# Kernel tuning notes

Measured on AMD Instinct MI355X. Metric: run time of the kernel, lower is better.

## Reference

```python
import jax, jax.numpy as jnp
import numpy as np

B, N, NP, NS = 8, 4096, 1024, 32
CF = 64            # input point-feature channels; in_channel = 3 + CF = 67
MLP = [64, 128, 256]
EPS = 1e-5         # BatchNorm eps (torch default)


def setup_inputs() -> dict:
    key = jax.random.key(0)
    ks = jax.random.split(key, 8)
    inp = {
        "xyz": jax.random.normal(ks[0], (B, N, 3), jnp.float32),
        "points": jax.random.normal(ks[1], (B, CF, N), jnp.float32),
        "sample_idx": jax.random.randint(ks[2], (B, NP), 0, N, dtype=jnp.int32),
        "neighbor_idx": jax.random.randint(ks[3], (B, NP, NS), 0, N, dtype=jnp.int32),
    }
    c = 3 + CF
    for i, o in enumerate(MLP):
        wk = jax.random.fold_in(ks[4], i)
        inp[f"W{i}"] = jax.random.normal(wk, (o, c), jnp.float32) * (1.0 / np.sqrt(c))
        inp[f"b{i}"] = jnp.zeros((o,), jnp.float32)
        inp[f"gamma{i}"] = jnp.ones((o,), jnp.float32)
        inp[f"beta{i}"] = jnp.zeros((o,), jnp.float32)
        c = o
    return inp


def _forward(xyz, points, sample_idx, neighbor_idx, params):
    # xyz: (B,N,3)  points: (B,CF,N)
    new_xyz = jnp.take_along_axis(xyz, sample_idx[:, :, None], axis=1)        # (B,NP,3)
    nbr_xyz = jax.vmap(lambda x, idx: x[idx])(xyz, neighbor_idx)               # (B,NP,NS,3)
    rel = nbr_xyz - new_xyz[:, :, None, :]                                     # (B,NP,NS,3)
    nbr_feat = jax.vmap(lambda f, idx: f[:, idx])(points, neighbor_idx)        # (B,CF,NP,NS)
    x = jnp.concatenate([rel.transpose(0, 3, 1, 2), nbr_feat], axis=1)         # (B,3+CF,NP,NS)
    # 1x1 Conv2d -> BatchNorm2d (training-mode batch stats) -> ReLU stack
    for W, b, g, be in params:
        x = jnp.einsum('oc,bcps->bops', W, x) + b[None, :, None, None]
        mu = x.mean(axis=(0, 2, 3), keepdims=True)
        var = x.var(axis=(0, 2, 3), keepdims=True)
        x = g[None, :, None, None] * (x - mu) * jax.lax.rsqrt(var + EPS) + be[None, :, None, None]
        x = jax.nn.relu(x)
    new_points = x.max(axis=-1)                                                # (B,C_out,NP)
    return new_xyz, new_points


def reference(xyz, points, sample_idx, neighbor_idx,
              W0, b0, gamma0, beta0,
              W1, b1, gamma1, beta1,
              W2, b2, gamma2, beta2):
    params = [(W0, b0, gamma0, beta0), (W1, b1, gamma1, beta1), (W2, b2, gamma2, beta2)]
    return _forward(xyz, points, sample_idx, neighbor_idx, params)
```

## Files before the change

kernel.cpp:

```cpp
#include <hip/hip_runtime.h>

typedef unsigned short u16;
typedef unsigned int u32;
typedef __attribute__((ext_vector_type(8))) short short8;
typedef __attribute__((ext_vector_type(16))) float f32x16;

#define BB 8
#define NN 4096
#define NPP 1024
#define NSS 32
#define CFF 64
#define C0 67
#define H0 64
#define H1 128
#define H2 256
#define MTOT (BB*NPP*NSS)
#define BN_EPS 1e-5f
#define INV_M (1.0f/262144.0f)

#define MFMA32(a,b,c) __builtin_amdgcn_mfma_f32_32x32x16_bf16(a,b,c,0,0,0)

__device__ __forceinline__ float bf2f(u16 h){ return __uint_as_float(((u32)h)<<16); }
__device__ __forceinline__ u16 f2bf(float f){
  u32 u = __float_as_uint(f);
  u32 r = (u + 0x7fffu + ((u>>16)&1u)) >> 16;
  return (u16)r;
}
__device__ __forceinline__ u32 pack2(float a, float b){
  return (u32)f2bf(a) | ((u32)f2bf(b)<<16);
}

#define WS_NEED 46280704u

__global__ __launch_bounds__(256) void k_setup(
    const float* __restrict__ xyz, const float* __restrict__ points,
    const int* __restrict__ sidx,
    const float* __restrict__ W0, const float* __restrict__ W1, const float* __restrict__ W2,
    u16* __restrict__ ptsT, u16* __restrict__ Wt0c, u16* __restrict__ Wt1c,
    u16* __restrict__ Wt2c, float* __restrict__ out_newxyz)
{
  int blk = blockIdx.x, tid = threadIdx.x;
  if (blk < 512) {
    __shared__ float t[64][65];
    int b = blk >> 6, n0 = (blk & 63) << 6;
    int nloc = tid & 63, cpart = tid >> 6;
    for (int i = 0; i < 16; ++i) {
      int c = i*4 + cpart;
      t[c][nloc] = points[(size_t)(b*CFF + c)*NN + n0 + nloc];
    }
    __syncthreads();
    int cloc = tid & 63, npart = tid >> 6;
    for (int i = 0; i < 16; ++i) {
      int n = i*4 + npart;
      ptsT[((size_t)(b*NN + n0 + n))*CFF + cloc] = f2bf(t[cloc][n]);
    }
  } else if (blk < 544) {
    int t0 = (blk - 512)*256 + tid;
    int b = t0 >> 10;
    int s = sidx[t0];
    for (int k = 0; k < 3; ++k)
      out_newxyz[(size_t)t0*3 + k] = xyz[((size_t)(b*NN + s))*3 + k];
  } else if (blk == 544) {
    for (int i = 0; i < 24; ++i) {
      int e = i*256 + tid;
      int kc = e >> 9, o = (e >> 3) & 63, j = e & 7, k = kc*8 + j;
      float v = (k < 64) ? W0[o*C0 + 3 + k] : ((k < 67) ? W0[o*C0 + (k - 64)] : 0.f);
      Wt0c[e] = f2bf(v);
    }
  } else if (blk == 545) {
    for (int i = 0; i < 32; ++i) {
      int e = i*256 + tid;
      int kc = e >> 10, n = (e >> 3) & 127, j = e & 7;
      Wt1c[e] = f2bf(W1[n*H0 + kc*8 + j]);
    }
  } else {
    int base = (blk - 546) * 4096;
    for (int i = 0; i < 16; ++i) {
      int e = base + i*256 + tid;
      int kc = e >> 11, n = (e >> 3) & 255, j = e & 7;
      Wt2c[e] = f2bf(W2[n*H1 + kc*8 + j]);
    }
  }
}

__global__ __launch_bounds__(256) void k_xyz_only(
    const float* __restrict__ xyz, const int* __restrict__ sidx, float* __restrict__ out_newxyz)
{
  int t0 = blockIdx.x*256 + threadIdx.x;
  int b = t0 >> 10;
  int s = sidx[t0];
  for (int k = 0; k < 3; ++k)
    out_newxyz[(size_t)t0*3 + k] = xyz[((size_t)(b*NN + s))*3 + k];
}

__global__ __launch_bounds__(256) void k_l0(
    const float* __restrict__ xyz, const int* __restrict__ sidx, const int* __restrict__ nidx,
    const u16* __restrict__ ptsT, const u16* __restrict__ Wt0c,
    u16* __restrict__ y0, float* __restrict__ stats)
{
  __shared__ u16 XLc[12*128*8];
  __shared__ u16 W0c[12*64*8];
  int tid = threadIdx.x;
  int m0 = blockIdx.x * 128;
  int b = m0 >> 15;

  for (int i = 0; i < 3; ++i)
    ((uint4*)W0c)[i*256 + tid] = ((const uint4*)Wt0c)[i*256 + tid];

  int pos = tid & 127, half = tid >> 7;
  int m = m0 + pos;
  int nb = nidx[m];
  {
    const uint4* prow = (const uint4*)(ptsT + ((size_t)(b*NN + nb))*CFF + half*32);
    uint4 h0 = prow[0], h1 = prow[1], h2 = prow[2], h3 = prow[3];
    *(uint4*)&XLc[((half*4+0)*128 + pos)*8] = h0;
    *(uint4*)&XLc[((half*4+1)*128 + pos)*8] = h1;
    *(uint4*)&XLc[((half*4+2)*128 + pos)*8] = h2;
    *(uint4*)&XLc[((half*4+3)*128 + pos)*8] = h3;
    if (half == 0) {
      int p = (m & 32767) >> 5;
      int sp = sidx[b*NPP + p];
      float r0 = xyz[((size_t)(b*NN+nb))*3+0] - xyz[((size_t)(b*NN+sp))*3+0];
      float r1 = xyz[((size_t)(b*NN+nb))*3+1] - xyz[((size_t)(b*NN+sp))*3+1];
      float r2 = xyz[((size_t)(b*NN+nb))*3+2] - xyz[((size_t)(b*NN+sp))*3+2];
      uint4 v = { pack2(r0, r1), pack2(r2, 0.f), 0u, 0u };
      *(uint4*)&XLc[(8*128 + pos)*8] = v;
    } else {
      uint4 z = {0u,0u,0u,0u};
      *(uint4*)&XLc[(9*128 + pos)*8]  = z;
      *(uint4*)&XLc[(10*128 + pos)*8] = z;
      *(uint4*)&XLc[(11*128 + pos)*8] = z;
    }
  }
  __syncthreads();

  int lane = tid & 63, wv = tid >> 6;
  int l31 = lane & 31, kh = lane >> 5;
  int nt = wv & 1, mtb = (wv >> 1) * 2;
  f32x16 acc[2];
  for (int mi = 0; mi < 2; ++mi) for (int r = 0; r < 16; ++r) acc[mi][r] = 0.f;

  for (int kt = 0; kt < 6; ++kt) {
    int ck = kt*2 + kh;
    short8 bfrag = *(const short8*)&W0c[(ck*64 + nt*32 + l31)*8];
    for (int mi = 0; mi < 2; ++mi) {
      short8 afrag = *(const short8*)&XLc[(ck*128 + (mtb+mi)*32 + l31)*8];
      acc[mi] = MFMA32(afrag, bfrag, acc[mi]);
    }
  }

  float s = 0.f, q = 0.f;
  for (int mi = 0; mi < 2; ++mi)
    for (int r = 0; r < 16; ++r) { float y = acc[mi][r]; s += y; q += y*y; }
  s += __shfl_xor(s, 32); q += __shfl_xor(q, 32);
  if (lane < 32) {
    int slot = blockIdx.x & 7;
    atomicAdd(&stats[slot*256 + nt*32 + lane], s);
    atomicAdd(&stats[2048 + slot*256 + nt*32 + lane], q);
  }
  for (int mi = 0; mi < 2; ++mi)
    for (int r = 0; r < 16; ++r) {
      int mm = (mtb+mi)*32 + (r&3) + 8*(r>>2) + 4*kh;
      y0[(size_t)(m0+mm)*H0 + nt*32 + l31] = f2bf(acc[mi][r]);
    }
}

__global__ __launch_bounds__(256) void k_l1s(
    const u16* __restrict__ y0, const u16* __restrict__ Wt1c,
    const float* __restrict__ g0, const float* __restrict__ e0,
    const float* __restrict__ stIn, float* __restrict__ stOut)
{
  __shared__ u16 X0c[8*128*8];
  __shared__ u16 W1c[8*128*8];
  __shared__ float scl0[64], sft0[64];
  int tid = threadIdx.x;
  int m0 = blockIdx.x * 128;

  if (tid < 64) {
    float s = 0.f, q = 0.f;
    for (int sl = 0; sl < 8; ++sl) { s += stIn[sl*256 + tid]; q += stIn[2048 + sl*256 + tid]; }
    float mu = s*INV_M, var = q*INV_M - mu*mu;
    float sc = g0[tid] * rsqrtf(var + BN_EPS);
    scl0[tid] = sc; sft0[tid] = e0[tid] - mu*sc;
  }
  for (int i = 0; i < 4; ++i)
    ((uint4*)W1c)[i*256 + tid] = ((const uint4*)Wt1c)[i*256 + tid];

  int pos = tid & 127, half = tid >> 7;
  {
    const u16* row = y0 + (size_t)(m0 + pos)*H0 + half*32;
    u16 hs[32];
    for (int t = 0; t < 4; ++t) *(uint4*)&hs[t*8] = ((const uint4*)row)[t];
    __syncthreads();
    u16 ob[32];
    for (int j = 0; j < 32; ++j) {
      int c = half*32 + j;
      ob[j] = f2bf(fmaxf(fmaf(scl0[c], bf2f(hs[j]), sft0[c]), 0.f));
    }
    for (int t = 0; t < 4; ++t)
      *(uint4*)&X0c[((half*4+t)*128 + pos)*8] = *(uint4*)&ob[t*8];
  }
  __syncthreads();

  int lane = tid & 63, wv = tid >> 6;
  int l31 = lane & 31, kh = lane >> 5;
  f32x16 acc[4];
  for (int mt = 0; mt < 4; ++mt) for (int r = 0; r < 16; ++r) acc[mt][r] = 0.f;

  for (int kt = 0; kt < 4; ++kt) {
    int ck = kt*2 + kh;
    short8 bfrag = *(const short8*)&W1c[(ck*128 + wv*32 + l31)*8];
    for (int mt = 0; mt < 4; ++mt) {
      short8 afrag = *(const short8*)&X0c[(ck*128 + mt*32 + l31)*8];
      acc[mt] = MFMA32(afrag, bfrag, acc[mt]);
    }
  }

  float s = 0.f, q = 0.f;
  for (int mt = 0; mt < 4; ++mt)
    for (int r = 0; r < 16; ++r) { float y = acc[mt][r]; s += y; q += y*y; }
  s += __shfl_xor(s, 32); q += __shfl_xor(q, 32);
  if (lane < 32) {
    int slot = blockIdx.x & 7;
    atomicAdd(&stOut[slot*256 + wv*32 + lane], s);
    atomicAdd(&stOut[2048 + slot*256 + wv*32 + lane], q);
  }
}

__global__ __launch_bounds__(256) void k_l2f(
    const u16* __restrict__ y0, const u16* __restrict__ Wt1c, const u16* __restrict__ Wt2c,
    const float* __restrict__ g0, const float* __restrict__ e0,
    const float* __restrict__ g1, const float* __restrict__ e1,
    const float* __restrict__ st0, const float* __restrict__ st1, float* __restrict__ stOut,
    u16* __restrict__ mxp, u16* __restrict__ mnp)
{
  __shared__ u16 X1c[16*64*8];
  __shared__ u16 UB[16384];
  __shared__ float scl0[64], sft0[64], scl1[128], sft1[128];
  int tid = threadIdx.x;
  int m0 = blockIdx.x * 64;

  if (tid < 64) {
    float s = 0.f, q = 0.f;
    for (int sl = 0; sl < 8; ++sl) { s += st0[sl*256 + tid]; q += st0[2048 + sl*256 + tid]; }
    float mu = s*INV_M, var = q*INV_M - mu*mu;
    float sc = g0[tid] * rsqrtf(var + BN_EPS);
    scl0[tid] = sc; sft0[tid] = e0[tid] - mu*sc;
  }
  if (tid < 128) {
    float s = 0.f, q = 0.f;
    for (int sl = 0; sl < 8; ++sl) { s += st1[sl*256 + tid]; q += st1[2048 + sl*256 + tid]; }
    float mu = s*INV_M, var = q*INV_M - mu*mu;
    float sc = g1[tid] * rsqrtf(var + BN_EPS);
    scl1[tid] = sc; sft1[tid] = e1[tid] - mu*sc;
  }
  u16* X0c = UB;
  u16* W1c = UB + 4096;
  for (int i = 0; i < 4; ++i)
    ((uint4*)W1c)[i*256 + tid] = ((const uint4*)Wt1c)[i*256 + tid];

  int pos = tid & 63, grp = tid >> 6;
  {
    const u16* row = y0 + (size_t)(m0 + pos)*H0 + grp*16;
    u16 hs[16];
    *(uint4*)&hs[0] = ((const uint4*)row)[0];
    *(uint4*)&hs[8] = ((const uint4*)row)[1];
    __syncthreads();
    u16 ob[16];
    for (int j = 0; j < 16; ++j) {
      int c = grp*16 + j;
      ob[j] = f2bf(fmaxf(fmaf(scl0[c], bf2f(hs[j]), sft0[c]), 0.f));
    }
    *(uint4*)&X0c[((2*grp)*64 + pos)*8]   = *(uint4*)&ob[0];
    *(uint4*)&X0c[((2*grp+1)*64 + pos)*8] = *(uint4*)&ob[8];
  }
  __syncthreads();

  int lane = tid & 63, wv = tid >> 6;
  int l31 = lane & 31, kh = lane >> 5;

  f32x16 acc1[2];
  for (int mt = 0; mt < 2; ++mt) for (int r = 0; r < 16; ++r) acc1[mt][r] = 0.f;
  for (int kt = 0; kt < 4; ++kt) {
    int ck = kt*2 + kh;
    short8 bfrag = *(const short8*)&W1c[(ck*128 + wv*32 + l31)*8];
    for (int mt = 0; mt < 2; ++mt) {
      short8 afrag = *(const short8*)&X0c[(ck*64 + mt*32 + l31)*8];
      acc1[mt] = MFMA32(afrag, bfrag, acc1[mt]);
    }
  }

  {
    int ch = wv*32 + l31;
    int cb = ch >> 3, cr = ch & 7;
    float sc1 = scl1[ch], sf1 = sft1[ch];
    for (int mt = 0; mt < 2; ++mt)
      for (int r = 0; r < 16; ++r) {
        int mm = mt*32 + (r&3) + 8*(r>>2) + 4*kh;
        X1c[(cb*64 + mm)*8 + cr] = f2bf(fmaxf(fmaf(sc1, acc1[mt][r], sf1), 0.f));
      }
  }
  __syncthreads();

  f32x16 acc2[2][2];
  for (int nt = 0; nt < 2; ++nt) for (int mt = 0; mt < 2; ++mt)
    for (int r = 0; r < 16; ++r) acc2[nt][mt][r] = 0.f;

  for (int h = 0; h < 2; ++h) {
    for (int i = 0; i < 8; ++i)
      ((uint4*)UB)[i*256 + tid] = ((const uint4*)Wt2c)[h*2048 + i*256 + tid];
    __syncthreads();
    for (int k4 = 0; k4 < 4; ++k4) {
      int ckx = (h*4 + k4)*2 + kh;
      int ckw = k4*2 + kh;
      short8 a[2], bf_[2];
      for (int mt = 0; mt < 2; ++mt) a[mt]  = *(const short8*)&X1c[(ckx*64 + mt*32 + l31)*8];
      for (int nt = 0; nt < 2; ++nt) bf_[nt] = *(const short8*)&UB[(ckw*256 + wv*64 + nt*32 + l31)*8];
      for (int nt = 0; nt < 2; ++nt)
        for (int mt = 0; mt < 2; ++mt)
          acc2[nt][mt] = MFMA32(a[mt], bf_[nt], acc2[nt][mt]);
    }
    __syncthreads();
  }

  int slot = blockIdx.x & 7;
  for (int nt = 0; nt < 2; ++nt) {
    float s = 0.f, q = 0.f;
    float mx[2] = {-3.0e38f, -3.0e38f}, mn[2] = {3.0e38f, 3.0e38f};
    for (int mt = 0; mt < 2; ++mt)
      for (int r = 0; r < 16; ++r) {
        float y = acc2[nt][mt][r];
        s += y; q += y*y;
        mx[mt] = fmaxf(mx[mt], y); mn[mt] = fminf(mn[mt], y);
      }
    s += __shfl_xor(s, 32); q += __shfl_xor(q, 32);
    mx[0] = fmaxf(mx[0], __shfl_xor(mx[0], 32));
    mx[1] = fmaxf(mx[1], __shfl_xor(mx[1], 32));
    mn[0] = fminf(mn[0], __shfl_xor(mn[0], 32));
    mn[1] = fminf(mn[1], __shfl_xor(mn[1], 32));
    if (lane < 32) {
      int c = wv*64 + nt*32 + lane;
      atomicAdd(&stOut[slot*256 + c], s);
      atomicAdd(&stOut[2048 + slot*256 + c], q);
      for (int mt = 0; mt < 2; ++mt) {
        size_t pr = (size_t)blockIdx.x*2 + mt;
        mxp[pr*H2 + c] = f2bf(mx[mt]);
        mnp[pr*H2 + c] = f2bf(mn[mt]);
      }
    }
  }
}

__global__ __launch_bounds__(256) void k_final(
    const u16* __restrict__ mxp, const u16* __restrict__ mnp,
    const float* __restrict__ gma, const float* __restrict__ bta,
    const float* __restrict__ stIn, float* __restrict__ out_np)
{
  __shared__ float tmp[256][33];
  int tid = threadIdx.x;
  int b = blockIdx.x >> 5;
  int p0 = (blockIdx.x & 31) * 32;

  float s = 0.f, q = 0.f;
  for (int sl = 0; sl < 8; ++sl) { s += stIn[sl*256 + tid]; q += stIn[2048 + sl*256 + tid]; }
  float mu = s*INV_M, var = q*INV_M - mu*mu;
  float sc = gma[tid] * rsqrtf(var + BN_EPS);
  float sh = bta[tid] - mu*sc;

  for (int pp = 0; pp < 32; ++pp) {
    size_t base = ((size_t)(b*NPP + p0 + pp))*H2 + tid;
    float xv = bf2f(mxp[base]), nv = bf2f(mnp[base]);
    float v = (sc >= 0.f) ? fmaf(sc, xv, sh) : fmaf(sc, nv, sh);
    tmp[tid][pp] = fmaxf(v, 0.f);
  }
  __syncthreads();

  int pl = tid & 31, cg = tid >> 5;
  for (int cc = 0; cc < 32; ++cc) {
    int c = cc*8 + cg;
    out_np[((size_t)b*H2 + c)*NPP + p0 + pl] = tmp[c][pl];
  }
}

extern "C" void kernel_launch(void* const* d_in, const int* in_sizes, int n_in,
                              void* d_out, int out_size, void* d_ws, size_t ws_size,
                              hipStream_t stream)
{
  const float* xyz    = (const float*)d_in[0];
  const float* points = (const float*)d_in[1];
  const int*   sidx   = (const int*)d_in[2];
  const int*   nidx   = (const int*)d_in[3];
  const float* W0 = (const float*)d_in[4];
  const float* g0 = (const float*)d_in[6];
  const float* e0 = (const float*)d_in[7];
  const float* W1 = (const float*)d_in[8];
  const float* g1 = (const float*)d_in[10];
  const float* e1 = (const float*)d_in[11];
  const float* W2 = (const float*)d_in[12];
  const float* g2 = (const float*)d_in[14];
  const float* e2 = (const float*)d_in[15];

  float* out_xyz = (float*)d_out;
  float* out_np  = out_xyz + (size_t)BB*NPP*3;

  if (ws_size < (size_t)WS_NEED) {
    hipMemsetAsync(out_np, 0, (size_t)BB*H2*NPP*4, stream);
    k_xyz_only<<<32, 256, 0, stream>>>(xyz, sidx, out_xyz);
    return;
  }

  char* ws = (char*)d_ws;
  float* stats = (float*)(ws + 0);
  u16*   Wt0c  = (u16*)(ws + 49152);
  u16*   Wt1c  = (u16*)(ws + 61440);
  u16*   Wt2c  = (u16*)(ws + 77824);
  u16*   ptsT  = (u16*)(ws + 143360);
  u16*   y0    = (u16*)(ws + 4337664);
  u16*   mxp   = (u16*)(ws + 37892096);
  u16*   mnp   = (u16*)(ws + 42086400);

  hipMemsetAsync(stats, 0, 3*4096*sizeof(float), stream);
  k_setup<<<554, 256, 0, stream>>>(xyz, points, sidx, W0, W1, W2,
                                   ptsT, Wt0c, Wt1c, Wt2c, out_xyz);
  k_l0<<<MTOT/128, 256, 0, stream>>>(xyz, sidx, nidx, ptsT, Wt0c, y0, stats);
  k_l1s<<<MTOT/128, 256, 0, stream>>>(y0, Wt1c, g0, e0, stats, stats + 4096);
  k_l2f<<<MTOT/64, 256, 0, stream>>>(y0, Wt1c, Wt2c, g0, e0, g1, e1,
                                     stats, stats + 4096, stats + 8192, mxp, mnp);
  k_final<<<256, 256, 0, stream>>>(mxp, mnp, g2, e2, stats + 8192, out_np);
}
```

Before: 177.6 us.

## Vectorize transposes, stage y0 stores via LDS, load weights directly into registers

The points transpose in setup now uses float4 loads and packed 16-byte bf16 stores. The layer-0 kernel stages its output tile in LDS with an XOR swizzle so y0 is written with coalesced 16-byte stores instead of scattered 2-byte stores. The layer-1 and layer-2 kernels skip staging weights through shared memory and load MFMA B fragments straight from global into registers. They also swizzle the X1 LDS layout to reduce bank conflicts and add occupancy hints to launch_bounds. The cost is more global weight traffic per block, which relies on L2 hits, and higher register pressure.

```diff
diff --git a/kernel.cpp b/kernel.cpp
--- a/kernel.cpp
+++ b/kernel.cpp
@@ -41,18 +41,22 @@
 {
   int blk = blockIdx.x, tid = threadIdx.x;
   if (blk < 512) {
-    __shared__ float t[64][65];
+    __shared__ float t[64][68];
     int b = blk >> 6, n0 = (blk & 63) << 6;
-    int nloc = tid & 63, cpart = tid >> 6;
-    for (int i = 0; i < 16; ++i) {
-      int c = i*4 + cpart;
-      t[c][nloc] = points[(size_t)(b*CFF + c)*NN + n0 + nloc];
+    for (int it = 0; it < 4; ++it) {
+      int u = it*256 + tid;
+      int nq = u & 15, c = u >> 4;
+      float4 v = *(const float4*)&points[(size_t)(b*CFF + c)*NN + n0 + nq*4];
+      *(float4*)&t[c][nq*4] = v;
     }
     __syncthreads();
-    int cloc = tid & 63, npart = tid >> 6;
-    for (int i = 0; i < 16; ++i) {
-      int n = i*4 + npart;
-      ptsT[((size_t)(b*NN + n0 + n))*CFF + cloc] = f2bf(t[cloc][n]);
+    for (int it = 0; it < 2; ++it) {
+      int u = it*256 + tid;
+      int oct = u & 7, n = u >> 3;
+      u16 pk[8];
+#pragma unroll
+      for (int j = 0; j < 8; ++j) pk[j] = f2bf(t[oct*8 + j][n]);
+      *(uint4*)&ptsT[((size_t)(b*NN + n0 + n))*CFF + oct*8] = *(uint4*)pk;
     }
   } else if (blk < 544) {
     int t0 = (blk - 512)*256 + tid;
@@ -158,23 +162,54 @@
     atomicAdd(&stats[slot*256 + nt*32 + lane], s);
     atomicAdd(&stats[2048 + slot*256 + nt*32 + lane], q);
   }
-  for (int mi = 0; mi < 2; ++mi)
-    for (int r = 0; r < 16; ++r) {
-      int mm = (mtb+mi)*32 + (r&3) + 8*(r>>2) + 4*kh;
-      y0[(size_t)(m0+mm)*H0 + nt*32 + l31] = f2bf(acc[mi][r]);
-    }
-}
-
-__global__ __launch_bounds__(256) void k_l1s(
+
+  __syncthreads();
+  {
+    int chx = (nt*32 + l31) ^ (kh*32);
+#pragma unroll
+    for (int mi = 0; mi < 2; ++mi)
+#pragma unroll
+      for (int r = 0; r < 16; ++r) {
+        int mm = (mtb+mi)*32 + (r&3) + 8*(r>>2) + 4*kh;
+        XLc[mm*64 + chx] = f2bf(acc[mi][r]);
+      }
+  }
+  __syncthreads();
+  {
+    uint4* dst = (uint4*)(y0 + (size_t)m0*H0);
+#pragma unroll
+    for (int i = 0; i < 4; ++i) {
+      int t16 = i*256 + tid;
+      int mrow = t16 >> 3, ch0 = (t16 & 7)*8;
+      int idx = mrow*64 + (ch0 ^ (32*((mrow>>2)&1)));
+      dst[t16] = *(const uint4*)&XLc[idx];
+    }
+  }
+}
+
+__global__ __launch_bounds__(256, 4) void k_l1s(
     const u16* __restrict__ y0, const u16* __restrict__ Wt1c,
     const float* __restrict__ g0, const float* __restrict__ e0,
     const float* __restrict__ stIn, float* __restrict__ stOut)
 {
   __shared__ u16 X0c[8*128*8];
-  __shared__ u16 W1c[8*128*8];
   __shared__ float scl0[64], sft0[64];
   int tid = threadIdx.x;
   int m0 = blockIdx.x * 128;
+  int lane = tid & 63, wv = tid >> 6;
+  int l31 = lane & 31, kh = lane >> 5;
+
+  int pos = tid & 127, half = tid >> 7;
+  u16 hs[32];
+  {
+    const u16* row = y0 + (size_t)(m0 + pos)*H0 + half*32;
+#pragma unroll
+    for (int t = 0; t < 4; ++t) *(uint4*)&hs[t*8] = ((const uint4*)row)[t];
+  }
+  short8 b1[4];
+#pragma unroll
+  for (int kt = 0; kt < 4; ++kt)
+    b1[kt] = *(const short8*)&Wt1c[((kt*2 + kh)*128 + wv*32 + l31)*8];
 
   if (tid < 64) {
     float s = 0.f, q = 0.f;
@@ -183,41 +218,39 @@
     float sc = g0[tid] * rsqrtf(var + BN_EPS);
     scl0[tid] = sc; sft0[tid] = e0[tid] - mu*sc;
   }
-  for (int i = 0; i < 4; ++i)
-    ((uint4*)W1c)[i*256 + tid] = ((const uint4*)Wt1c)[i*256 + tid];
-
-  int pos = tid & 127, half = tid >> 7;
-  {
-    const u16* row = y0 + (size_t)(m0 + pos)*H0 + half*32;
-    u16 hs[32];
-    for (int t = 0; t < 4; ++t) *(uint4*)&hs[t*8] = ((const uint4*)row)[t];
-    __syncthreads();
+  __syncthreads();
+
+  {
     u16 ob[32];
+#pragma unroll
     for (int j = 0; j < 32; ++j) {
       int c = half*32 + j;
       ob[j] = f2bf(fmaxf(fmaf(scl0[c], bf2f(hs[j]), sft0[c]), 0.f));
     }
+#pragma unroll
     for (int t = 0; t < 4; ++t)
       *(uint4*)&X0c[((half*4+t)*128 + pos)*8] = *(uint4*)&ob[t*8];
   }
   __syncthreads();
 
-  int lane = tid & 63, wv = tid >> 6;
-  int l31 = lane & 31, kh = lane >> 5;
   f32x16 acc[4];
+#pragma unroll
   for (int mt = 0; mt < 4; ++mt) for (int r = 0; r < 16; ++r) acc[mt][r] = 0.f;
 
+#pragma unroll
   for (int kt = 0; kt < 4; ++kt) {
     int ck = kt*2 + kh;
-    short8 bfrag = *(const short8*)&W1c[(ck*128 + wv*32 + l31)*8];
+#pragma unroll
     for (int mt = 0; mt < 4; ++mt) {
       short8 afrag = *(const short8*)&X0c[(ck*128 + mt*32 + l31)*8];
-      acc[mt] = MFMA32(afrag, bfrag, acc[mt]);
+      acc[mt] = MFMA32(afrag, b1[kt], acc[mt]);
     }
   }
 
   float s = 0.f, q = 0.f;
+#pragma unroll
   for (int mt = 0; mt < 4; ++mt)
+#pragma unroll
     for (int r = 0; r < 16; ++r) { float y = acc[mt][r]; s += y; q += y*y; }
   s += __shfl_xor(s, 32); q += __shfl_xor(q, 32);
   if (lane < 32) {
@@ -227,18 +260,32 @@
   }
 }
 
-__global__ __launch_bounds__(256) void k_l2f(
+__global__ __launch_bounds__(256, 4) void k_l2f(
     const u16* __restrict__ y0, const u16* __restrict__ Wt1c, const u16* __restrict__ Wt2c,
     const float* __restrict__ g0, const float* __restrict__ e0,
     const float* __restrict__ g1, const float* __restrict__ e1,
     const float* __restrict__ st0, const float* __restrict__ st1, float* __restrict__ stOut,
     u16* __restrict__ mxp, u16* __restrict__ mnp)
 {
+  __shared__ u16 X0c[8*64*8];
   __shared__ u16 X1c[16*64*8];
-  __shared__ u16 UB[16384];
   __shared__ float scl0[64], sft0[64], scl1[128], sft1[128];
   int tid = threadIdx.x;
   int m0 = blockIdx.x * 64;
+  int lane = tid & 63, wv = tid >> 6;
+  int l31 = lane & 31, kh = lane >> 5;
+
+  int pos = tid & 63, grp = tid >> 6;
+  u16 hs[16];
+  {
+    const u16* row = y0 + (size_t)(m0 + pos)*H0 + grp*16;
+    *(uint4*)&hs[0] = ((const uint4*)row)[0];
+    *(uint4*)&hs[8] = ((const uint4*)row)[1];
+  }
+  short8 b1[4];
+#pragma unroll
+  for (int kt = 0; kt < 4; ++kt)
+    b1[kt] = *(const short8*)&Wt1c[((kt*2 + kh)*128 + wv*32 + l31)*8];
 
   if (tid < 64) {
     float s = 0.f, q = 0.f;
@@ -254,19 +301,11 @@
     float sc = g1[tid] * rsqrtf(var + BN_EPS);
     scl1[tid] = sc; sft1[tid] = e1[tid] - mu*sc;
   }
-  u16* X0c = UB;
-  u16* W1c = UB + 4096;
-  for (int i = 0; i < 4; ++i)
-    ((uint4*)W1c)[i*256 + tid] = ((const uint4*)Wt1c)[i*256 + tid];
-
-  int pos = tid & 63, grp = tid >> 6;
-  {
-    const u16* row = y0 + (size_t)(m0 + pos)*H0 + grp*16;
-    u16 hs[16];
-    *(uint4*)&hs[0] = ((const uint4*)row)[0];
-    *(uint4*)&hs[8] = ((const uint4*)row)[1];
-    __syncthreads();
+  __syncthreads();
+
+  {
     u16 ob[16];
+#pragma unroll
     for (int j = 0; j < 16; ++j) {
       int c = grp*16 + j;
       ob[j] = f2bf(fmaxf(fmaf(scl0[c], bf2f(hs[j]), sft0[c]), 0.f));
@@ -276,58 +315,65 @@
   }
   __syncthreads();
 
-  int lane = tid & 63, wv = tid >> 6;
-  int l31 = lane & 31, kh = lane >> 5;
-
   f32x16 acc1[2];
+#pragma unroll
   for (int mt = 0; mt < 2; ++mt) for (int r = 0; r < 16; ++r) acc1[mt][r] = 0.f;
+#pragma unroll
   for (int kt = 0; kt < 4; ++kt) {
     int ck = kt*2 + kh;
-    short8 bfrag = *(const short8*)&W1c[(ck*128 + wv*32 + l31)*8];
+#pragma unroll
     for (int mt = 0; mt < 2; ++mt) {
       short8 afrag = *(const short8*)&X0c[(ck*64 + mt*32 + l31)*8];
-      acc1[mt] = MFMA32(afrag, bfrag, acc1[mt]);
-    }
-  }
-
-  {
-    int ch = wv*32 + l31;
-    int cb = ch >> 3, cr = ch & 7;
-    float sc1 = scl1[ch], sf1 = sft1[ch];
+      acc1[mt] = MFMA32(afrag, b1[kt], acc1[mt]);
+    }
+  }
+
+  {
+    int ch1 = wv*32 + l31;
+    int cb = ch1 >> 3, cr = ch1 & 7, sw = cb & 3;
+    float sc1 = scl1[ch1], sf1 = sft1[ch1];
+#pragma unroll
     for (int mt = 0; mt < 2; ++mt)
+#pragma unroll
       for (int r = 0; r < 16; ++r) {
         int mm = mt*32 + (r&3) + 8*(r>>2) + 4*kh;
-        X1c[(cb*64 + mm)*8 + cr] = f2bf(fmaxf(fmaf(sc1, acc1[mt][r], sf1), 0.f));
+        X1c[(cb*64 + (mm ^ sw))*8 + cr] = f2bf(fmaxf(fmaf(sc1, acc1[mt][r], sf1), 0.f));
       }
   }
   __syncthreads();
 
   f32x16 acc2[2][2];
+#pragma unroll
   for (int nt = 0; nt < 2; ++nt) for (int mt = 0; mt < 2; ++mt)
     for (int r = 0; r < 16; ++r) acc2[nt][mt][r] = 0.f;
 
-  for (int h = 0; h < 2; ++h) {
-    for (int i = 0; i < 8; ++i)
-      ((uint4*)UB)[i*256 + tid] = ((const uint4*)Wt2c)[h*2048 + i*256 + tid];
-    __syncthreads();
-    for (int k4 = 0; k4 < 4; ++k4) {
-      int ckx = (h*4 + k4)*2 + kh;
-      int ckw = k4*2 + kh;
-      short8 a[2], bf_[2];
-      for (int mt = 0; mt < 2; ++mt) a[mt]  = *(const short8*)&X1c[(ckx*64 + mt*32 + l31)*8];
-      for (int nt = 0; nt < 2; ++nt) bf_[nt] = *(const short8*)&UB[(ckw*256 + wv*64 + nt*32 + l31)*8];
-      for (int nt = 0; nt < 2; ++nt)
-        for (int mt = 0; mt < 2; ++mt)
-          acc2[nt][mt] = MFMA32(a[mt], bf_[nt], acc2[nt][mt]);
-    }
-    __syncthreads();
+#pragma unroll
+  for (int k4 = 0; k4 < 8; ++k4) {
+    int ck = k4*2 + kh;
+    int sw = ck & 3;
+    short8 bf_[2];
+#pragma unroll
+    for (int nt = 0; nt < 2; ++nt)
+      bf_[nt] = *(const short8*)&Wt2c[(ck*256 + wv*64 + nt*32 + l31)*8];
+    short8 a[2];
+#pragma unroll
+    for (int mt = 0; mt < 2; ++mt)
+      a[mt] = *(const short8*)&X1c[(ck*64 + ((mt*32 + l31) ^ sw))*8];
+#pragma unroll
+    for (int nt = 0; nt < 2; ++nt)
+#pragma unroll
+      for (int mt = 0; mt < 2; ++mt)
+        acc2[nt][mt] = MFMA32(a[mt], bf_[nt], acc2[nt][mt]);
   }
 
   int slot = blockIdx.x & 7;
+#pragma unroll
   for (int nt = 0; nt < 2; ++nt) {
     float s = 0.f, q = 0.f;
     float mx[2] = {-3.0e38f, -3.0e38f}, mn[2] = {3.0e38f, 3.0e38f};
+#pragma unroll
     for (int mt = 0; mt < 2; ++mt)
+#pragma unroll
       for (int r = 0; r < 16; ++r) {
         float y = acc2[nt][mt][r];
         s += y; q += y*y;
@@ -342,6 +388,7 @@
       int c = wv*64 + nt*32 + lane;
       atomicAdd(&stOut[slot*256 + c], s);
       atomicAdd(&stOut[2048 + slot*256 + c], q);
+#pragma unroll
       for (int mt = 0; mt < 2; ++mt) {
         size_t pr = (size_t)blockIdx.x*2 + mt;
         mxp[pr*H2 + c] = f2bf(mx[mt]);
```

Result: faster. 170.5 us (-4.0%).
